# Kernel optimization log

Measured on AMD Instinct MI355X. Metric: run time of the kernel, lower is better.

## Reference

```python
import jax, jax.numpy as jnp
import numpy as np

B, T, D = 64, 64, 64
E, HA, HB, OUT = 128, 128, 128, 1
SHORT = 2


def _rn(k, shape, scale=0.05):
    return jax.random.normal(k, shape, dtype=jnp.float32) * scale


def setup_inputs() -> dict:
    key = jax.random.key(0)
    ks = jax.random.split(key, 18)
    return {
        "x": jax.random.normal(ks[0], (B, T, D), dtype=jnp.float32),
        "W_emb": _rn(ks[1], (E, D)), "b_emb": _rn(ks[2], (E,)),
        "Wi_a": _rn(ks[3], (3 * HA, E)), "Wh_a": _rn(ks[4], (3 * HA, HA)),
        "bi_a": _rn(ks[5], (3 * HA,)), "bh_a": _rn(ks[6], (3 * HA,)),
        "Wi_b": _rn(ks[7], (3 * HB, E)), "Wh_b": _rn(ks[8], (3 * HB, HB)),
        "bi_b": _rn(ks[9], (3 * HB,)), "bh_b": _rn(ks[10], (3 * HB,)),
        "Wa": _rn(ks[11], (1, HA)), "ba": _rn(ks[12], (1,)),
        "Wb": _rn(ks[13], (E, HB)), "bb": _rn(ks[14], (E,)),
        "Wo": _rn(ks[15], (OUT, E)), "bo": _rn(ks[16], (OUT,)),
        "short": SHORT,
    }


def _gru_cell(x, h, Wi, Wh, bi, bh):
    # PyTorch GRU cell: gates ordered (r, z, n)
    gi = x @ Wi.T + bi
    gh = h @ Wh.T + bh
    ir, iz, in_ = jnp.split(gi, 3, axis=-1)
    hr, hz, hn = jnp.split(gh, 3, axis=-1)
    r = jax.nn.sigmoid(ir + hr)
    z = jax.nn.sigmoid(iz + hz)
    n = jnp.tanh(in_ + r * hn)
    return (1.0 - z) * n + z * h


def _forward(x, W_emb, b_emb, Wi_a, Wh_a, bi_a, bh_a, Wi_b, Wh_b, bi_b, bh_b,
             Wa, ba, Wb, bb, Wo, bo, short):
    Bn, Tn = x.shape[0], x.shape[1]
    temp = jnp.transpose(x, (1, 0, 2))            # [T, B, D]
    emb = temp @ W_emb.T + b_emb                  # [T, B, E]
    P = Tn - 1                                    # prefix p handles att_timesteps t = p+1
    S = Tn - 1                                    # max reversed-prefix length
    p_idx = jnp.arange(P)
    h0a = jnp.zeros((P, Bn, Wh_a.shape[1]), x.dtype)
    h0b = jnp.zeros((P, Bn, Wh_b.shape[1]), x.dtype)

    # All prefixes at once: for prefix p, reversed input at step s is emb[p - s].
    def step(carry, s):
        ha, hb = carry
        j = jnp.clip(p_idx - s, 0, Tn - 1)        # [P]
        e_in = emb[j]                             # [P, B, E]
        x_in = temp[j]                            # [P, B, D]
        na = _gru_cell(e_in, ha, Wi_a, Wh_a, bi_a, bh_a)
        nb = _gru_cell(e_in, hb, Wi_b, Wh_b, bi_b, bh_b)
        valid = (p_idx >= s)[:, None, None]
        ha = jnp.where(valid, na, ha)
        hb = jnp.where(valid, nb, hb)
        return (ha, hb), (ha, hb, e_in, x_in)

    _, (Ha, Hb, Eg, Xg) = jax.lax.scan(step, (h0a, h0b), jnp.arange(S))
    Ha = 0.5 * Ha                                 # reverse_h_a * 0.5, [S, P, B, HA]
    Hb = 0.5 * Hb                                 # reverse_h_b * 0.5, [S, P, B, HB]

    mask = p_idx[None, :] >= jnp.arange(S)[:, None]   # [S, P] valid scan steps
    preA = jnp.einsum('spbh,h->spb', Ha, Wa[0]) + ba[0]
    preA = jnp.where(mask[:, :, None], preA, -jnp.inf)
    alpha = jax.nn.softmax(preA, axis=0)              # softmax over prefix positions
    beta = jnp.tanh(jnp.einsum('spbh,eh->spbe', Hb, Wb) + bb)  # [S, P, B, E]

    # context: c[p] = sum_s alpha * beta * emb[p-s]  (softmax is order-invariant)
    c = jnp.einsum('spb,spbe->pbe', alpha, beta * Eg)          # [P, B, E]
    pred = c @ Wo.T + bo                                        # [P, B, 1]

    # interpretability weights: e = (beta * w_out) @ W_emb, f = alpha*e*x, g = mean over prefix
    e_chain = jnp.einsum('spbe,ed->spbd', beta * Wo[0], W_emb)  # [S, P, B, D]
    f = alpha[..., None] * e_chain * Xg
    g = jnp.sum(f, axis=0) / (p_idx[:, None, None] + 1.0)       # mean over t = p+1 steps

    pred = jnp.transpose(pred[short + 1:], (1, 0, 2))           # [B, T-2-short, 1]
    weight = jnp.transpose(g[short + 1:], (1, 0, 2))            # [B, T-2-short, D]
    return pred, weight


def reference(x, W_emb, b_emb, Wi_a, Wh_a, bi_a, bh_a, Wi_b, Wh_b, bi_b, bh_b,
              Wa, ba, Wb, bb, Wo, bo, short):
    return _forward(x, W_emb, b_emb, Wi_a, Wh_a, bi_a, bh_a, Wi_b, Wh_b, bi_b,
                    bh_b, Wa, ba, Wb, bb, Wo, bo, short)
```

## Files before the change

kernel.cpp:

```cpp
#include <hip/hip_runtime.h>
#include <hip/hip_bf16.h>
#include <math.h>

#define B_ 64
#define T_ 64
#define D_ 64
#define PMIN 3
#define NPOUT 60
#define NCHUNK 4

#define LOG2E     1.4426950408889634f
#define TWOLOG2E  2.8853900817779268f

typedef __hip_bfloat16 bf16;
typedef __attribute__((ext_vector_type(4))) short s16x4;
typedef __attribute__((ext_vector_type(8))) short s16x8;
typedef __attribute__((ext_vector_type(4))) float f32x4;

#define OFF_EMB   0
#define OFF_WIC2  524288
#define OFF_XT    622592
#define OFF_GIPK  884736
#define OFF_WPK   2457600
#define OFF_BPPK  2506752
#define OFF_WMPK  2514944
#define OFF_WALPK 2519040
#define OFF_FLAG  2520064

__device__ __forceinline__ float bf2f(unsigned short u) {
    union { float f; unsigned u32; } x; x.u32 = ((unsigned)u) << 16; return x.f;
}
__device__ __forceinline__ unsigned short f2bf(float f) {
    union { float f; unsigned u; } x; x.f = f;
    unsigned r = x.u + 0x7FFFu + ((x.u >> 16) & 1u);
    return (unsigned short)(r >> 16);
}
__device__ __forceinline__ float LDF(const void* p, int i, int flag) {
    return flag ? ((const float*)p)[i] : bf2f(((const unsigned short*)p)[i]);
}
__device__ __forceinline__ float sig2(float xneg) {
    return __builtin_amdgcn_rcpf(1.f + __builtin_exp2f(xneg));
}
__device__ __forceinline__ float tanh2(float x2) {
    return 1.f - 2.f * __builtin_amdgcn_rcpf(1.f + __builtin_exp2f(x2));
}
__device__ __forceinline__ int kpi(int s) {
    return (s & ~31) | ((s & 1) << 4) | ((s & 31) >> 1);
}

__global__ void detect_dtype(const unsigned short* xr, int* flag)
{
    int tid = threadIdx.x;
    int bad = 0;
    for (int i = tid; i < 4096; i += 256) {
        int ex = (xr[i] >> 7) & 0xFF;
        if (ex >= 140) bad++;
    }
    __shared__ int s[256];
    s[tid] = bad;
    __syncthreads();
    for (int st = 128; st > 0; st >>= 1) {
        if (tid < st) s[tid] += s[tid + st];
        __syncthreads();
    }
    if (tid == 0) *flag = (s[0] > 4) ? 1 : 0;
}

__global__ void prep_all(const void* p_x, const void* p_wemb,
                         const void* p_wia, const void* p_wib,
                         const void* p_wha, const void* p_whb,
                         const void* p_wa, const void* p_wb, const void* p_wo,
                         float* ws, const int* flagp)
{
    const int flag = *flagp;
    int id = blockIdx.x * 256 + threadIdx.x;
    if (id < 98304) {
        float v = (id < 49152) ? LDF(p_wia, id, flag)
                               : LDF(p_wib, id - 49152, flag);
        ws[OFF_WIC2 + id] = v;
    } else if (id < 360448) {
        int id5 = id - 98304;
        int b = id5 & 63, d = (id5 >> 6) & 63, t = id5 >> 12;
        ws[OFF_XT + id5] = LDF(p_x, (b * 64 + t) * 64 + d, flag);
    } else if (id < 458752) {
        unsigned short* wpk = (unsigned short*)(ws + OFF_WPK);
        int id3 = id - 360448;
        int w = id3 / 12288, r1 = id3 % 12288;
        int nt = r1 / 2048, r2 = r1 % 2048;
        int kt = r2 / 512, r3 = r2 % 512;
        int lane = r3 >> 3, j = r3 & 7;
        int cell = w >> 2, wv = w & 3;
        int gate = nt >> 1, tt = nt & 1;
        int g = gate * 128 + wv * 32 + tt * 16 + (lane & 15);
        int k = kpi(kt * 32 + (lane >> 4) * 8 + j);
        float sc = (gate < 2) ? -LOG2E : TWOLOG2E;
        wpk[id3] = f2bf(sc * LDF(cell ? p_whb : p_wha, g * 128 + k, flag));
    } else if (id < 475136) {
        unsigned short* bpk = (unsigned short*)(ws + OFF_BPPK);
        int id4 = id - 458752;
        int w = id4 / 2048, r = id4 % 2048;
        int kt = r / 512, lane = (r % 512) >> 3, j = r & 7;
        int e = w * 16 + (lane & 15);
        int k = kpi(kt * 32 + (lane >> 4) * 8 + j);
        bpk[id4] = f2bf(LOG2E * LDF(p_wb, e * 128 + k, flag));
    } else if (id < 483328) {
        unsigned short* wmk = (unsigned short*)(ws + OFF_WMPK);
        int id6 = id - 475136;
        int nt = id6 / 2048, r = id6 % 2048;
        int kt = r / 512, lane = (r % 512) >> 3, j = r & 7;
        int d = nt * 16 + (lane & 15);
        int e = kt * 32 + (lane >> 4) * 8 + j;
        wmk[id6] = f2bf(LDF(p_wo, e, flag) * LDF(p_wemb, e * 64 + d, flag));
    } else {
        unsigned short* alk = (unsigned short*)(ws + OFF_WALPK);
        int id7 = id - 483328;
        int kt = id7 / 512, lane = (id7 % 512) >> 3, j = id7 & 7;
        int k = kpi(kt * 32 + (lane >> 4) * 8 + j);
        alk[id7] = ((lane & 15) == 0) ? f2bf(0.5f * LOG2E * LDF(p_wa, k, flag))
                                      : (unsigned short)0;
    }
}

__global__ void prep_gi(float* ws, const void* p_x, const void* p_wemb,
                        const void* p_bemb, const void* p_bia, const void* p_bha,
                        const void* p_bib, const void* p_bhb, const int* flagp)
{
    const int flag = *flagp;
    unsigned short* gipk = (unsigned short*)(ws + OFF_GIPK);
    int t = blockIdx.x >> 3;
    int chunk = blockIdx.x & 7;
    int b0 = chunk * 8;
    int tid = threadIdx.x;
    __shared__ __align__(16) float sX[8][64];
    __shared__ __align__(16) float sWe[128][64];
    __shared__ __align__(16) float semT2[8][132];
    __shared__ __align__(16) unsigned short stg[6144];

    for (int i = tid; i < 512; i += 256) {
        int r = i >> 6, d = i & 63;
        sX[r][d] = LDF(p_x, ((b0 + r) * 64 + t) * 64 + d, flag);
    }
    for (int i = tid; i < 8192; i += 256)
        sWe[i >> 6][i & 63] = LDF(p_wemb, i, flag);
    __syncthreads();

    #pragma unroll
    for (int q = 0; q < 4; q++) {
        int o = tid + q * 256;
        int e = o & 127, r = o >> 7;
        float acc = LDF(p_bemb, e, flag);
        #pragma unroll
        for (int d = 0; d < 64; d += 4) {
            f32x4 xv = *(const f32x4*)&sX[r][d];
            f32x4 wv = *(const f32x4*)&sWe[e][d];
            acc += xv[0]*wv[0] + xv[1]*wv[1] + xv[2]*wv[2] + xv[3]*wv[3];
        }
        semT2[r][e] = acc;
        ws[OFF_EMB + (size_t)((t * 64 + b0 + r) * 128) + e] = acc;
    }
    __syncthreads();

    float acc3[3][8];
    #pragma unroll
    for (int g3 = 0; g3 < 3; g3++)
        #pragma unroll
        for (int r = 0; r < 8; r++) acc3[g3][r] = 0.f;
    const float* w2 = ws + OFF_WIC2;
    #pragma unroll 2
    for (int e0 = 0; e0 < 128; e0 += 4) {
        f32x4 wv0 = *(const f32x4*)(w2 + (size_t)(tid      ) * 128 + e0);
        f32x4 wv1 = *(const f32x4*)(w2 + (size_t)(tid + 256) * 128 + e0);
        f32x4 wv2 = *(const f32x4*)(w2 + (size_t)(tid + 512) * 128 + e0);
        f32x4 h[8];
        #pragma unroll
        for (int r = 0; r < 8; r++) h[r] = *(const f32x4*)&semT2[r][e0];
        #pragma unroll
        for (int r = 0; r < 8; r++)
            #pragma unroll
            for (int c = 0; c < 4; c++) {
                acc3[0][r] += wv0[c] * h[r][c];
                acc3[1][r] += wv1[c] * h[r][c];
                acc3[2][r] += wv2[c] * h[r][c];
            }
    }
    #pragma unroll
    for (int g3 = 0; g3 < 3; g3++) {
        int g = tid + g3 * 256;
        int cellg = g / 384, gr = g % 384;
        int gate = gr / 128, kh = gr % 128;
        int wvp = kh / 32, tt2 = (kh % 32) / 16, l15p = kh % 16;
        int wq = cellg * 4 + wvp;
        float bias = LDF(cellg ? p_bib : p_bia, gr, flag);
        if (gate < 2) bias += LDF(cellg ? p_bhb : p_bha, gr, flag);
        float sc = (gate < 2) ? -LOG2E : TWOLOG2E;
        #pragma unroll
        for (int r = 0; r < 8; r++) {
            float v = sc * (acc3[g3][r] + bias);
            int lane2 = (r >> 2) * 16 + l15p;
            int slot = gate * 8 + tt2 * 4 + (r & 3);
            stg[(wq * 32 + lane2) * 24 + slot] = f2bf(v);
        }
    }
    __syncthreads();
    const uint4* s4 = (const uint4*)stg;
    const int c16 = chunk >> 1, rhalf = chunk & 1;
    uint4* d4 = (uint4*)(gipk + (size_t)(t * 4 + c16) * 12288);
    for (int i = tid; i < 768; i += 256) {
        int wq = i / 96, rem = i % 96;
        d4[wq * 192 + rhalf * 96 + rem] = s4[i];
    }
}


__launch_bounds__(512, 2)
__global__ void chain_kernel(const float* ws, void* outv, const int* flagp,
                             const void* p_bha, const void* p_bhb,
                             const void* p_bb, const void* p_ba,
                             const void* p_bo, const void* p_wo)
{
    const int p = PMIN + (NPOUT - 1) - (int)blockIdx.x / NCHUNK;
    const int chunk = (int)blockIdx.x % NCHUNK;
    const int tid = threadIdx.x;
    const int lane = tid & 63;
    const int w = tid >> 6;
    const int cell = w >> 2;
    const int wv = w & 3;
    const int l15 = lane & 15;
    const int quad = lane >> 4;

    __shared__ __align__(16) short hbf[2][2][16][136];
    __shared__ __align__(16) short betbf[2][16][136];
    __shared__ __align__(16) short sWm[4][4][64][8];
    __shared__ float spaLds[2][16];

    const unsigned short* gipk = (const unsigned short*)(ws + OFF_GIPK);
    const unsigned short* wpk  = (const unsigned short*)(ws + OFF_WPK);
    const unsigned short* bpk  = (const unsigned short*)(ws + OFF_BPPK);
    const unsigned short* alk  = (const unsigned short*)(ws + OFF_WALPK);
    const int flag = *flagp;

    {
        const int* s2 = (const int*)(ws + OFF_WMPK);
        int* d2 = (int*)&sWm[0][0][0][0];
        for (int i = tid; i < 4096; i += 512) d2[i] = s2[i];
        int* hz = (int*)&hbf[0][0][0][0];
        for (int i = tid; i < 4352; i += 512) hz[i] = 0;
        int* bz = (int*)&betbf[0][0][0];
        for (int i = tid; i < 2176; i += 512) bz[i] = 0;
    }

    s16x8 wB[6][4];
    #pragma unroll
    for (int nt = 0; nt < 6; nt++)
        #pragma unroll
        for (int kt = 0; kt < 4; kt++)
            wB[nt][kt] = *(const s16x8*)(wpk + (((w * 6 + nt) * 4 + kt) * 64 + lane) * 8);
    s16x8 bBp[4], wAl[4];
    #pragma unroll
    for (int kt = 0; kt < 4; kt++) {
        bBp[kt] = *(const s16x8*)(bpk + ((w * 4 + kt) * 64 + lane) * 8);
        wAl[kt] = *(const s16x8*)(alk + (kt * 64 + lane) * 8);
    }

    const float bhnS0 = TWOLOG2E *
        LDF(cell ? p_bhb : p_bha, 256 + wv * 32 + l15, flag);
    const float bhnS1 = TWOLOG2E *
        LDF(cell ? p_bhb : p_bha, 256 + wv * 32 + 16 + l15, flag);
    const float bbE2 = TWOLOG2E * LDF(p_bb, w * 16 + l15, flag);
    const float bafS = LOG2E * LDF(p_ba, 0, flag);
    const float bof  = LDF(p_bo, 0, flag);

    float h_old[8];
    #pragma unroll
    for (int i = 0; i < 8; i++) h_old[i] = 0.f;
    float accR[9];
    #pragma unroll
    for (int i = 0; i < 9; i++) accR[i] = 0.f;

    __syncthreads();

    for (int it = 0; it <= p + 1; it++) {
        const int j = p - it;
        const int jp = j + 1;
        const bool doGru = (j >= 0);
        const bool doAcc = (it > 0);
        const int cur = it & 1;
        const int nxt = cur ^ 1;
        const int dbuf = it & 1;

        s16x8 giv[3];
        if (doGru) {
            const unsigned short* gp0 =
                gipk + ((((size_t)j * 4 + chunk) * 8 + w) * 64 + lane) * 24;
            giv[0] = *(const s16x8*)(gp0);
            giv[1] = *(const s16x8*)(gp0 + 8);
            giv[2] = *(const s16x8*)(gp0 + 16);
        }
        f32x4 xv, em0, em1;
        if (doAcc) {
            if (w < 4) {
                xv = *(const f32x4*)(ws + OFF_XT + ((size_t)jp * 64 + w * 16 + l15) * 64
                                     + chunk * 16 + quad * 4);
            } else {
                const int row = quad * 4 + (w - 4);
                const float* ep = ws + OFF_EMB
                                  + ((size_t)jp * 64 + chunk * 16 + row) * 128 + l15 * 8;
                em0 = *(const f32x4*)ep;
                em1 = *(const f32x4*)(ep + 4);
            }
        }

        f32x4 Cg[6], Cbp, Cal;
        #pragma unroll
        for (int nt = 0; nt < 6; nt++) Cg[nt] = (f32x4){0.f,0.f,0.f,0.f};
        Cbp = (f32x4){0.f,0.f,0.f,0.f};
        Cal = (f32x4){0.f,0.f,0.f,0.f};

        #pragma unroll
        for (int kt = 0; kt < 4; kt++) {
            s16x8 aB = *(const s16x8*)&hbf[cur][1][l15][kt * 32 + quad * 8];
            s16x8 aA;
            if (cell == 0 || w == 7) aA = *(const s16x8*)&hbf[cur][0][l15][kt * 32 + quad * 8];
            else aA = aB;
            s16x8 aOwn = cell ? aB : aA;
            #pragma unroll
            for (int nt = 0; nt < 6; nt++)
                Cg[nt] = __builtin_amdgcn_mfma_f32_16x16x32_bf16(aOwn, wB[nt][kt], Cg[nt], 0, 0, 0);
            Cbp = __builtin_amdgcn_mfma_f32_16x16x32_bf16(aB, bBp[kt], Cbp, 0, 0, 0);
            if (w == 7)
                Cal = __builtin_amdgcn_mfma_f32_16x16x32_bf16(aA, wAl[kt], Cal, 0, 0, 0);
        }

        if (w == 7 && l15 == 0) {
            #pragma unroll
            for (int reg = 0; reg < 4; reg++)
                spaLds[dbuf][quad * 4 + reg] = fminf(Cal[reg] + bafS, 86.f);
        }
        if (doGru) {
            #pragma unroll
            for (int reg = 0; reg < 4; reg++) {
                float rr0 = sig2(bf2f((unsigned short)giv[0][reg]) + Cg[0][reg]);
                float zz0 = sig2(bf2f((unsigned short)giv[1][reg]) + Cg[2][reg]);
                float nn0 = tanh2(bf2f((unsigned short)giv[2][reg])
                                  + rr0 * (Cg[4][reg] + bhnS0));
                float h0 = (1.f - zz0) * nn0 + zz0 * h_old[reg];
                h_old[reg] = h0;
                float rr1 = sig2(bf2f((unsigned short)giv[0][4 + reg]) + Cg[1][reg]);
                float zz1 = sig2(bf2f((unsigned short)giv[1][4 + reg]) + Cg[3][reg]);
                float nn1 = tanh2(bf2f((unsigned short)giv[2][4 + reg])
                                  + rr1 * (Cg[5][reg] + bhnS1));
                float h1 = (1.f - zz1) * nn1 + zz1 * h_old[4 + reg];
                h_old[4 + reg] = h1;
                unsigned pk;
                asm("v_cvt_pk_bf16_f32 %0, %1, %2" : "=v"(pk) : "v"(h0), "v"(h1));
                *(unsigned*)&hbf[nxt][cell][quad * 4 + reg][wv * 32 + l15 * 2] = pk;
            }
        }
        {
            #pragma unroll
            for (int reg = 0; reg < 4; reg++) {
                float bv = tanh2(Cbp[reg] + bbE2);
                betbf[dbuf][quad * 4 + reg][w * 16 + l15] = (short)f2bf(bv);
            }
        }

        __syncthreads();

        if (doAcc) {
            if (w < 4) {
                f32x4 ec = (f32x4){0.f,0.f,0.f,0.f};
                #pragma unroll
                for (int kt = 0; kt < 4; kt++) {
                    s16x8 a = *(const s16x8*)&betbf[dbuf][l15][kt * 32 + quad * 8];
                    s16x8 bw = *(const s16x8*)&sWm[w][kt][lane][0];
                    ec = __builtin_amdgcn_mfma_f32_16x16x32_bf16(a, bw, ec, 0, 0, 0);
                }
                #pragma unroll
                for (int reg = 0; reg < 4; reg++) {
                    float we = __builtin_exp2f(spaLds[dbuf][quad * 4 + reg]);
                    accR[4 + reg] += we;
                    accR[reg] += we * ec[reg] * xv[reg];
                }
            } else {
                const int row = quad * 4 + (w - 4);
                float we = __builtin_exp2f(spaLds[dbuf][row]);
                accR[8] += we;
                const short* bp2 = &betbf[dbuf][row][l15 * 8];
                s16x4 blo = *(const s16x4*)bp2;
                s16x4 bhi = *(const s16x4*)(bp2 + 4);
                #pragma unroll
                for (int v = 0; v < 4; v++)
                    accR[v] += we * bf2f((unsigned short)blo[v]) * em0[v];
                #pragma unroll
                for (int v = 0; v < 4; v++)
                    accR[4 + v] += we * bf2f((unsigned short)bhi[v]) * em1[v];
            }
        }
    }

    if (w >= 4) {
        const int row = quad * 4 + (w - 4);
        float wo8[8];
        if (flag) {
            const float* wp = (const float*)p_wo + l15 * 8;
            #pragma unroll
            for (int v = 0; v < 8; v++) wo8[v] = wp[v];
        } else {
            const unsigned short* wp = (const unsigned short*)p_wo + l15 * 8;
            #pragma unroll
            for (int v = 0; v < 8; v++) wo8[v] = bf2f(wp[v]);
        }
        float part = 0.f;
        #pragma unroll
        for (int v = 0; v < 8; v++) part += accR[v] * wo8[v];
        part += __shfl_xor(part, 1);
        part += __shfl_xor(part, 2);
        part += __shfl_xor(part, 4);
        part += __shfl_xor(part, 8);
        if (l15 == 0) {
            int bglob = chunk * 16 + row;
            float pr = part / accR[8] + bof;
            size_t oi = (size_t)bglob * NPOUT + (p - PMIN);
            if (flag) ((float*)outv)[oi] = pr;
            else      ((bf16*)outv)[oi] = __float2bfloat16(pr);
        }
    } else {
        const float invt = 1.f / (float)(p + 1);
        #pragma unroll
        for (int reg = 0; reg < 4; reg++) {
            int row = quad * 4 + reg;
            int bglob = chunk * 16 + row;
            float gv = accR[reg] / accR[4 + reg] * invt;
            size_t oi = (size_t)B_ * NPOUT
                      + ((size_t)bglob * NPOUT + (p - PMIN)) * 64 + w * 16 + l15;
            if (flag) ((float*)outv)[oi] = gv;
            else      ((bf16*)outv)[oi] = __float2bfloat16(gv);
        }
    }
}

extern "C" void kernel_launch(void* const* d_in, const int* in_sizes, int n_in,
                              void* d_out, int out_size, void* d_ws, size_t ws_size,
                              hipStream_t stream)
{
    float* ws = (float*)d_ws;
    int* flagp = (int*)(ws + OFF_FLAG);

    hipLaunchKernelGGL(detect_dtype, dim3(1), dim3(256), 0, stream,
                       (const unsigned short*)d_in[0], flagp);
    hipLaunchKernelGGL(prep_all, dim3(1896), dim3(256), 0, stream,
                       d_in[0], d_in[1], d_in[3], d_in[7], d_in[4], d_in[8],
                       d_in[11], d_in[13], d_in[15], ws, flagp);
    hipLaunchKernelGGL(prep_gi, dim3(512), dim3(256), 0, stream,
                       ws, d_in[0], d_in[1], d_in[2], d_in[5], d_in[6],
                       d_in[9], d_in[10], flagp);
    hipLaunchKernelGGL(chain_kernel, dim3(NPOUT * NCHUNK), dim3(512), 0, stream,
                       ws, d_out, flagp,
                       d_in[6], d_in[10], d_in[14], d_in[12], d_in[16], d_in[15]);
}
```

Before: 318.9 us.

## Defer accumulation phase by one iteration to overlap with next GRU step

The accumulation phase (beta·W_emb MFMA plus weighted sums) now runs at the start of the next loop iteration on the other double buffer, instead of after the barrier in the same iteration. Its x/emb loads are held in registers across the iteration, and a final call drains the last stage after the loop. The exp2 of the attention logit is computed once by the writer lane rather than by every consumer thread. The intent is to let the accumulation overlap with the next step's gate MFMAs and shorten the serial recurrence per step, at the cost of higher register pressure and a reliance on the double-buffer indexing staying correct.

```diff
diff --git a/kernel.cpp b/kernel.cpp
--- a/kernel.cpp
+++ b/kernel.cpp
@@ -231,7 +231,7 @@
     __shared__ __align__(16) short hbf[2][2][16][136];
     __shared__ __align__(16) short betbf[2][16][136];
     __shared__ __align__(16) short sWm[4][4][64][8];
-    __shared__ float spaLds[2][16];
+    __shared__ float weLds[2][16];
 
     const unsigned short* gipk = (const unsigned short*)(ws + OFF_GIPK);
     const unsigned short* wpk  = (const unsigned short*)(ws + OFF_WPK);
@@ -277,13 +277,47 @@
     #pragma unroll
     for (int i = 0; i < 9; i++) accR[i] = 0.f;
 
+    f32x4 xvP = (f32x4){0.f,0.f,0.f,0.f};
+    f32x4 em0P = (f32x4){0.f,0.f,0.f,0.f};
+    f32x4 em1P = (f32x4){0.f,0.f,0.f,0.f};
+
+    auto phaseC = [&](int dbufP) {
+        if (w < 4) {
+            f32x4 ec = (f32x4){0.f,0.f,0.f,0.f};
+            #pragma unroll
+            for (int kt = 0; kt < 4; kt++) {
+                s16x8 a = *(const s16x8*)&betbf[dbufP][l15][kt * 32 + quad * 8];
+                s16x8 bw = *(const s16x8*)&sWm[w][kt][lane][0];
+                ec = __builtin_amdgcn_mfma_f32_16x16x32_bf16(a, bw, ec, 0, 0, 0);
+            }
+            #pragma unroll
+            for (int reg = 0; reg < 4; reg++) {
+                float we = weLds[dbufP][quad * 4 + reg];
+                accR[4 + reg] += we;
+                accR[reg] += we * ec[reg] * xvP[reg];
+            }
+        } else {
+            const int row = quad * 4 + (w - 4);
+            float we = weLds[dbufP][row];
+            accR[8] += we;
+            const short* bp2 = &betbf[dbufP][row][l15 * 8];
+            s16x4 blo = *(const s16x4*)bp2;
+            s16x4 bhi = *(const s16x4*)(bp2 + 4);
+            #pragma unroll
+            for (int v = 0; v < 4; v++)
+                accR[v] += we * bf2f((unsigned short)blo[v]) * em0P[v];
+            #pragma unroll
+            for (int v = 0; v < 4; v++)
+                accR[4 + v] += we * bf2f((unsigned short)bhi[v]) * em1P[v];
+        }
+    };
+
     __syncthreads();
 
     for (int it = 0; it <= p + 1; it++) {
         const int j = p - it;
         const int jp = j + 1;
         const bool doGru = (j >= 0);
-        const bool doAcc = (it > 0);
         const int cur = it & 1;
         const int nxt = cur ^ 1;
         const int dbuf = it & 1;
@@ -296,17 +330,19 @@
             giv[1] = *(const s16x8*)(gp0 + 8);
             giv[2] = *(const s16x8*)(gp0 + 16);
         }
-        f32x4 xv, em0, em1;
-        if (doAcc) {
+
+        if (it > 1) phaseC(dbuf ^ 1);
+
+        if (it > 0) {
             if (w < 4) {
-                xv = *(const f32x4*)(ws + OFF_XT + ((size_t)jp * 64 + w * 16 + l15) * 64
-                                     + chunk * 16 + quad * 4);
+                xvP = *(const f32x4*)(ws + OFF_XT + ((size_t)jp * 64 + w * 16 + l15) * 64
+                                      + chunk * 16 + quad * 4);
             } else {
                 const int row = quad * 4 + (w - 4);
                 const float* ep = ws + OFF_EMB
                                   + ((size_t)jp * 64 + chunk * 16 + row) * 128 + l15 * 8;
-                em0 = *(const f32x4*)ep;
-                em1 = *(const f32x4*)(ep + 4);
+                em0P = *(const f32x4*)ep;
+                em1P = *(const f32x4*)(ep + 4);
             }
         }
 
@@ -334,7 +370,8 @@
         if (w == 7 && l15 == 0) {
             #pragma unroll
             for (int reg = 0; reg < 4; reg++)
-                spaLds[dbuf][quad * 4 + reg] = fminf(Cal[reg] + bafS, 86.f);
+                weLds[dbuf][quad * 4 + reg] =
+                    __builtin_exp2f(fminf(Cal[reg] + bafS, 86.f));
         }
         if (doGru) {
             #pragma unroll
@@ -365,38 +402,9 @@
         }
 
         __syncthreads();
-
-        if (doAcc) {
-            if (w < 4) {
-                f32x4 ec = (f32x4){0.f,0.f,0.f,0.f};
-                #pragma unroll
-                for (int kt = 0; kt < 4; kt++) {
-                    s16x8 a = *(const s16x8*)&betbf[dbuf][l15][kt * 32 + quad * 8];
-                    s16x8 bw = *(const s16x8*)&sWm[w][kt][lane][0];
-                    ec = __builtin_amdgcn_mfma_f32_16x16x32_bf16(a, bw, ec, 0, 0, 0);
-                }
-                #pragma unroll
-                for (int reg = 0; reg < 4; reg++) {
-                    float we = __builtin_exp2f(spaLds[dbuf][quad * 4 + reg]);
-                    accR[4 + reg] += we;
-                    accR[reg] += we * ec[reg] * xv[reg];
-                }
-            } else {
-                const int row = quad * 4 + (w - 4);
-                float we = __builtin_exp2f(spaLds[dbuf][row]);
-                accR[8] += we;
-                const short* bp2 = &betbf[dbuf][row][l15 * 8];
-                s16x4 blo = *(const s16x4*)bp2;
-                s16x4 bhi = *(const s16x4*)(bp2 + 4);
-                #pragma unroll
-                for (int v = 0; v < 4; v++)
-                    accR[v] += we * bf2f((unsigned short)blo[v]) * em0[v];
-                #pragma unroll
-                for (int v = 0; v < 4; v++)
-                    accR[4 + v] += we * bf2f((unsigned short)bhi[v]) * em1[v];
-            }
-        }
-    }
+    }
+
+    phaseC((p + 1) & 1);
 
     if (w >= 4) {
         const int row = quad * 4 + (w - 4);
```

After: 315.9 us. Within noise of the previous version (-0.9%).
